# Kernel optimization log

Measured on AMD Instinct MI355X. Metric: run time of the kernel, lower is better.

The kernel has to match this reference:

```python
import jax, jax.numpy as jnp
import numpy as np

LN_EPS = 1e-5
MASK_FILL = -1e9


def setup_inputs() -> dict:
    key = jax.random.key(0)
    ks = jax.random.split(key, 8)
    B, S, D = 32, 1024, 1280
    Dout = 1280
    emb = jax.random.normal(ks[0], (B, S, D), dtype=jnp.float32)
    mask = jnp.ones((B, S), dtype=jnp.int32)
    w = 0.02
    return {
        "embeddings": emb,
        "attention_mask": mask,
        "Wq": jax.random.normal(ks[1], (D, D), jnp.float32) * w,
        "bq": jnp.zeros((D,), jnp.float32),
        "Wk": jax.random.normal(ks[2], (D, D), jnp.float32) * w,
        "bk": jnp.zeros((D,), jnp.float32),
        "Wv": jax.random.normal(ks[3], (D, D), jnp.float32) * w,
        "bv": jnp.zeros((D,), jnp.float32),
        "Wo": jax.random.normal(ks[4], (Dout, D), jnp.float32) * w,
        "bo": jnp.zeros((Dout,), jnp.float32),
        "gamma": jnp.ones((Dout,), jnp.float32),
        "beta": jnp.zeros((Dout,), jnp.float32),
    }


def reference(embeddings, attention_mask, Wq, bq, Wk, bk, Wv, bv, Wo, bo, gamma, beta):
    # Original torch module computes full [B,S,S] self-attention but only
    # consumes context[:, 0, :]. Mathematically identical (same output and
    # same gradients) to computing attention for query row 0 only.
    B, S, D = embeddings.shape
    scale = D ** -0.5
    q0 = embeddings[:, 0, :] @ Wq.T + bq                      # [B, D]
    k = jnp.einsum("bsd,ed->bse", embeddings, Wk) + bk        # [B, S, D]
    v = jnp.einsum("bsd,ed->bse", embeddings, Wv) + bv        # [B, S, D]
    scores = jnp.einsum("bd,bsd->bs", q0, k) * scale          # [B, S]
    scores = jnp.where(attention_mask == 0, MASK_FILL, scores)
    weights = jax.nn.softmax(scores, axis=-1)                 # [B, S]
    ctx = jnp.einsum("bs,bsd->bd", weights, v)                # [B, D]
    # output projection: Linear -> LayerNorm -> ReLU (dropout = identity in eval)
    h = ctx @ Wo.T + bo                                       # [B, Dout]
    mu = jnp.mean(h, axis=-1, keepdims=True)
    var = jnp.mean(jnp.square(h - mu), axis=-1, keepdims=True)
    h = (h - mu) * jax.lax.rsqrt(var + LN_EPS) * gamma + beta
    return jax.nn.relu(h)
```

## Files before the change

### kernel.cpp

```cpp
#include <hip/hip_runtime.h>

constexpr int cB = 32;
constexpr int cS = 1024;
constexpr int cD = 1280;
constexpr int KC = 16;
constexpr int NKC = cD / KC;
constexpr int NNC = cD / 256;

#define LN_EPS 1e-5f
#define MASK_FILL -1e9f
#define SCALE 0.02795084971874737f

__global__ __launch_bounds__(256) void k_dotT(const float* __restrict__ A,
                                              size_t lda,
                                              const float* __restrict__ W,
                                              const float* __restrict__ bias,
                                              float* __restrict__ out) {
    int w = threadIdx.x >> 6, lane = threadIdx.x & 63;
    int gw = blockIdx.x * 4 + w;
    int n = gw >> 1;
    int bh = (gw & 1) * 16;
    int d0 = lane * 4;

    float4 wr[5];
#pragma unroll
    for (int it = 0; it < 5; ++it)
        wr[it] = *reinterpret_cast<const float4*>(W + (size_t)n * cD + it * 256 + d0);
    float bn = bias[n];

#pragma unroll
    for (int bi = 0; bi < 16; ++bi) {
        int b = bh + bi;
        const float* a = A + (size_t)b * lda + d0;
        float4 av[5];
#pragma unroll
        for (int it = 0; it < 5; ++it)
            av[it] = *reinterpret_cast<const float4*>(a + it * 256);
        float dot = 0.f;
#pragma unroll
        for (int it = 0; it < 5; ++it)
            dot += av[it].x * wr[it].x + av[it].y * wr[it].y
                 + av[it].z * wr[it].z + av[it].w * wr[it].w;
#pragma unroll
        for (int off = 32; off; off >>= 1) dot += __shfl_xor(dot, off, 64);
        if (lane == 0) out[b * cD + n] = dot + bn;
    }
}

__global__ __launch_bounds__(256) void k_mm_p1(const float* __restrict__ A,
                                               const float* __restrict__ B,
                                               float* __restrict__ part) {
    int t = threadIdx.x;
    int nc = blockIdx.x % NNC, kc = blockIdx.x / NNC;
    int n0 = nc * 256, k0 = kc * KC;

    float w[KC];
#pragma unroll
    for (int kk = 0; kk < KC; ++kk)
        w[kk] = B[(size_t)(k0 + kk) * cD + n0 + t];

#pragma unroll
    for (int b = 0; b < cB; ++b) {
        const float* Ab = A + (size_t)b * cD + k0;
        float a0 = 0.f, a1 = 0.f, a2 = 0.f, a3 = 0.f;
#pragma unroll
        for (int kk = 0; kk < KC; kk += 4) {
            a0 += Ab[kk + 0] * w[kk + 0];
            a1 += Ab[kk + 1] * w[kk + 1];
            a2 += Ab[kk + 2] * w[kk + 2];
            a3 += Ab[kk + 3] * w[kk + 3];
        }
        part[(size_t)kc * (cB * cD) + b * cD + n0 + t] = (a0 + a1) + (a2 + a3);
    }
}

__global__ __launch_bounds__(256) void k_mm_red_qb(const float* __restrict__ part,
                                                   const float* __restrict__ q0,
                                                   const float* __restrict__ bk,
                                                   float* __restrict__ qk,
                                                   float* __restrict__ qb) {
    if (blockIdx.x < 160) {
        int i = blockIdx.x * 256 + threadIdx.x;
        float s = 0.f;
#pragma unroll
        for (int c = 0; c < NKC; ++c) s += part[(size_t)c * (cB * cD) + i];
        qk[i] = s;
    } else {
        int w = threadIdx.x >> 6, lane = threadIdx.x & 63;
        int d0 = lane * 4;
        float4 bkr[5];
#pragma unroll
        for (int it = 0; it < 5; ++it)
            bkr[it] = *reinterpret_cast<const float4*>(bk + it * 256 + d0);
#pragma unroll
        for (int r = 0; r < 8; ++r) {
            int b = w * 8 + r;
            float dot = 0.f;
#pragma unroll
            for (int it = 0; it < 5; ++it) {
                float4 qv = *reinterpret_cast<const float4*>(q0 + b * cD + it * 256 + d0);
                dot += qv.x * bkr[it].x + qv.y * bkr[it].y
                     + qv.z * bkr[it].z + qv.w * bkr[it].w;
            }
#pragma unroll
            for (int off = 32; off; off >>= 1) dot += __shfl_xor(dot, off, 64);
            if (lane == 0) qb[b] = dot;
        }
    }
}

__global__ __launch_bounds__(256) void k_attn(const float* __restrict__ emb,
                                              const float* __restrict__ qk,
                                              const float* __restrict__ qb,
                                              const int* __restrict__ mask,
                                              float* __restrict__ pm,
                                              float* __restrict__ pl,
                                              float* __restrict__ pacc) {
    __shared__ float s_all[4][cD];
    __shared__ float s_m[4], s_l[4];
    int blk = blockIdx.x;
    int b = blk >> 5, sc = blk & 31;
    int w = threadIdx.x >> 6, lane = threadIdx.x & 63;
    int d0 = lane * 4;

    float4 qkr[5];
#pragma unroll
    for (int it = 0; it < 5; ++it)
        qkr[it] = *reinterpret_cast<const float4*>(qk + b * cD + it * 256 + d0);
    float qbv = qb[b];

    float m = -INFINITY, l = 0.f;
    float4 acc[5];
#pragma unroll
    for (int it = 0; it < 5; ++it) acc[it] = make_float4(0.f, 0.f, 0.f, 0.f);

    int s0 = sc * 32 + w * 8;
    const float* ebase = emb + (size_t)(b * cS + s0) * cD + d0;

#define ATTN_ROW(rIdx, er)                                                     \
    {                                                                          \
        int s = s0 + (rIdx);                                                   \
        float dot = 0.f;                                                       \
        _Pragma("unroll")                                                      \
        for (int it = 0; it < 5; ++it)                                         \
            dot += er[it].x * qkr[it].x + er[it].y * qkr[it].y                 \
                 + er[it].z * qkr[it].z + er[it].w * qkr[it].w;                \
        _Pragma("unroll")                                                      \
        for (int off = 32; off; off >>= 1) dot += __shfl_xor(dot, off, 64);    \
        float scv = (mask[b * cS + s] == 0) ? MASK_FILL : (dot + qbv) * SCALE; \
        if (scv > m) {                                                         \
            float f = __expf(m - scv);                                         \
            l *= f;                                                            \
            _Pragma("unroll")                                                  \
            for (int it = 0; it < 5; ++it) {                                   \
                acc[it].x *= f; acc[it].y *= f;                                \
                acc[it].z *= f; acc[it].w *= f;                                \
            }                                                                  \
            m = scv;                                                           \
        }                                                                      \
        float p = __expf(scv - m);                                             \
        l += p;                                                                \
        _Pragma("unroll")                                                      \
        for (int it = 0; it < 5; ++it) {                                       \
            acc[it].x += p * er[it].x; acc[it].y += p * er[it].y;              \
            acc[it].z += p * er[it].z; acc[it].w += p * er[it].w;              \
        }                                                                      \
    }

    float4 erA[5], erB[5];
#pragma unroll
    for (int it = 0; it < 5; ++it)
        erA[it] = *reinterpret_cast<const float4*>(ebase + it * 256);

#pragma unroll
    for (int rr = 0; rr < 8; rr += 2) {
#pragma unroll
        for (int it = 0; it < 5; ++it)
            erB[it] = *reinterpret_cast<const float4*>(
                ebase + (size_t)(rr + 1) * cD + it * 256);
        ATTN_ROW(rr, erA);
        if (rr + 2 < 8) {
#pragma unroll
            for (int it = 0; it < 5; ++it)
                erA[it] = *reinterpret_cast<const float4*>(
                    ebase + (size_t)(rr + 2) * cD + it * 256);
        }
        ATTN_ROW(rr + 1, erB);
    }
#undef ATTN_ROW

    if (lane == 0) { s_m[w] = m; s_l[w] = l; }
    __syncthreads();
    float M = fmaxf(fmaxf(s_m[0], s_m[1]), fmaxf(s_m[2], s_m[3]));
    float f = __expf(m - M);
#pragma unroll
    for (int it = 0; it < 5; ++it)
        *reinterpret_cast<float4*>(&s_all[w][it * 256 + d0]) =
            make_float4(acc[it].x * f, acc[it].y * f, acc[it].z * f, acc[it].w * f);
    __syncthreads();

    if (threadIdx.x == 0) {
        float lt = s_l[0] * __expf(s_m[0] - M) + s_l[1] * __expf(s_m[1] - M)
                 + s_l[2] * __expf(s_m[2] - M) + s_l[3] * __expf(s_m[3] - M);
        pm[blk] = M; pl[blk] = lt;
    }
#pragma unroll
    for (int j = 0; j < 5; ++j) {
        int d = j * 256 + threadIdx.x;
        pacc[(size_t)blk * cD + d] =
            s_all[0][d] + s_all[1][d] + s_all[2][d] + s_all[3][d];
    }
}

__global__ __launch_bounds__(256) void k_attn_red(const float* __restrict__ pm,
                                                  const float* __restrict__ pl,
                                                  const float* __restrict__ pacc,
                                                  float* __restrict__ ectx) {
    int b = blockIdx.x / 5, j = blockIdx.x % 5;
    int d = j * 256 + threadIdx.x;
    float M = -INFINITY;
    for (int i = 0; i < 32; ++i) M = fmaxf(M, pm[b * 32 + i]);
    float L = 0.f, a = 0.f;
    for (int i = 0; i < 32; ++i) {
        float wf = __expf(pm[b * 32 + i] - M);
        L += pl[b * 32 + i] * wf;
        a += wf * pacc[(size_t)(b * 32 + i) * cD + d];
    }
    ectx[b * cD + d] = a / L;
}

__global__ __launch_bounds__(256) void k_ln(const float* __restrict__ h,
                                            const float* __restrict__ gamma,
                                            const float* __restrict__ beta,
                                            float* __restrict__ out) {
    int b = blockIdx.x;
    __shared__ float red[8];
    int wid = threadIdx.x >> 6, lane = threadIdx.x & 63;
    float v[5];
    float sum = 0.f;
#pragma unroll
    for (int j = 0; j < 5; ++j) {
        v[j] = h[b * cD + threadIdx.x + 256 * j];
        sum += v[j];
    }
#pragma unroll
    for (int off = 32; off; off >>= 1) sum += __shfl_xor(sum, off, 64);
    if (lane == 0) red[wid] = sum;
    __syncthreads();
    float mu = (red[0] + red[1] + red[2] + red[3]) * (1.f / cD);
    float vs = 0.f;
#pragma unroll
    for (int j = 0; j < 5; ++j) { float t = v[j] - mu; vs += t * t; }
#pragma unroll
    for (int off = 32; off; off >>= 1) vs += __shfl_xor(vs, off, 64);
    if (lane == 0) red[4 + wid] = vs;
    __syncthreads();
    float var = (red[4] + red[5] + red[6] + red[7]) * (1.f / cD);
    float inv = rsqrtf(var + LN_EPS);
#pragma unroll
    for (int j = 0; j < 5; ++j) {
        int idx = threadIdx.x + 256 * j;
        float o = (v[j] - mu) * inv * gamma[idx] + beta[idx];
        out[b * cD + idx] = fmaxf(o, 0.f);
    }
}

extern "C" void kernel_launch(void* const* d_in, const int* in_sizes, int n_in,
                              void* d_out, int out_size, void* d_ws, size_t ws_size,
                              hipStream_t stream) {
    const float* emb   = (const float*)d_in[0];
    const int*   mask  = (const int*)d_in[1];
    const float* Wq    = (const float*)d_in[2];
    const float* bq    = (const float*)d_in[3];
    const float* Wk    = (const float*)d_in[4];
    const float* bk    = (const float*)d_in[5];
    const float* Wv    = (const float*)d_in[6];
    const float* bv    = (const float*)d_in[7];
    const float* Wo    = (const float*)d_in[8];
    const float* bo    = (const float*)d_in[9];
    const float* gamma = (const float*)d_in[10];
    const float* beta  = (const float*)d_in[11];

    float* ws   = (float*)d_ws;
    float* part = ws;
    float* q0   = part + NKC * cB * cD;
    float* qk   = q0 + cB * cD;
    float* qb   = qk + cB * cD;
    float* pm   = qb + cB;
    float* pl   = pm + 1024;
    float* pacc = pl + 1024;
    float* ectx = pacc + (size_t)1024 * cD;
    float* ctx  = ectx + cB * cD;
    float* h    = ctx + cB * cD;

    k_dotT<<<640, 256, 0, stream>>>(emb, (size_t)cS * cD, Wq, bq, q0);
    k_mm_p1<<<NNC * NKC, 256, 0, stream>>>(q0, Wk, part);
    k_mm_red_qb<<<161, 256, 0, stream>>>(part, q0, bk, qk, qb);
    k_attn<<<cB * 32, 256, 0, stream>>>(emb, qk, qb, mask, pm, pl, pacc);
    k_attn_red<<<160, 256, 0, stream>>>(pm, pl, pacc, ectx);
    k_dotT<<<640, 256, 0, stream>>>(ectx, (size_t)cD, Wv, bv, ctx);
    k_dotT<<<640, 256, 0, stream>>>(ctx, (size_t)cD, Wo, bo, h);
    k_ln<<<cB, 256, 0, stream>>>(h, gamma, beta, (float*)d_out);
}
```

Measured before the change: 345.2 us.

## Replace split-K q·Wk partial GEMM with direct per-output kernel; batch shuffle reductions

Merges the split-K partial-sum kernel and its reduction into one kernel where each thread computes a full K=1280 dot product for one (batch, column) of q0·Wk. This removes the large partial buffer (80×32×1280 floats) along with its write and readback, and drops one launch. The cost is lower parallelism: only 160 blocks, each running a long serial loop over strided Wk rows. It also batches the warp-shuffle reductions across the 16 and 8 rows in k_dotT and the qb path for more ILP, and adds unroll pragmas in k_attn_red.

Measured after the change: 346.1 us. Within noise of the previous version (+0.3%).

```diff
diff --git a/kernel.cpp b/kernel.cpp
--- a/kernel.cpp
+++ b/kernel.cpp
@@ -3,8 +3,6 @@
 constexpr int cB = 32;
 constexpr int cS = 1024;
 constexpr int cD = 1280;
-constexpr int KC = 16;
-constexpr int NKC = cD / KC;
 constexpr int NNC = cD / 256;
 
 #define LN_EPS 1e-5f
@@ -28,6 +26,7 @@
         wr[it] = *reinterpret_cast<const float4*>(W + (size_t)n * cD + it * 256 + d0);
     float bn = bias[n];
 
+    float dot[16];
 #pragma unroll
     for (int bi = 0; bi < 16; ++bi) {
         int b = bh + bi;
@@ -36,55 +35,50 @@
 #pragma unroll
         for (int it = 0; it < 5; ++it)
             av[it] = *reinterpret_cast<const float4*>(a + it * 256);
-        float dot = 0.f;
+        float d = 0.f;
 #pragma unroll
         for (int it = 0; it < 5; ++it)
-            dot += av[it].x * wr[it].x + av[it].y * wr[it].y
-                 + av[it].z * wr[it].z + av[it].w * wr[it].w;
-#pragma unroll
-        for (int off = 32; off; off >>= 1) dot += __shfl_xor(dot, off, 64);
-        if (lane == 0) out[b * cD + n] = dot + bn;
-    }
-}
-
-__global__ __launch_bounds__(256) void k_mm_p1(const float* __restrict__ A,
-                                               const float* __restrict__ B,
-                                               float* __restrict__ part) {
-    int t = threadIdx.x;
-    int nc = blockIdx.x % NNC, kc = blockIdx.x / NNC;
-    int n0 = nc * 256, k0 = kc * KC;
-
-    float w[KC];
-#pragma unroll
-    for (int kk = 0; kk < KC; ++kk)
-        w[kk] = B[(size_t)(k0 + kk) * cD + n0 + t];
-
-#pragma unroll
-    for (int b = 0; b < cB; ++b) {
-        const float* Ab = A + (size_t)b * cD + k0;
+            d += av[it].x * wr[it].x + av[it].y * wr[it].y
+               + av[it].z * wr[it].z + av[it].w * wr[it].w;
+        dot[bi] = d;
+    }
+#pragma unroll
+    for (int off = 32; off; off >>= 1)
+#pragma unroll
+        for (int bi = 0; bi < 16; ++bi)
+            dot[bi] += __shfl_xor(dot[bi], off, 64);
+    if (lane == 0) {
+#pragma unroll
+        for (int bi = 0; bi < 16; ++bi)
+            out[(bh + bi) * cD + n] = dot[bi] + bn;
+    }
+}
+
+__global__ __launch_bounds__(256) void k_qk(const float* __restrict__ q0,
+                                            const float* __restrict__ Wk,
+                                            const float* __restrict__ bk,
+                                            float* __restrict__ qk,
+                                            float* __restrict__ qb) {
+    if (blockIdx.x < 160) {
+        int b = blockIdx.x / NNC, nc = blockIdx.x % NNC;
+        int n = nc * 256 + threadIdx.x;
+        const float* Ab = q0 + (size_t)b * cD;
+        const float* Wp = Wk + n;
         float a0 = 0.f, a1 = 0.f, a2 = 0.f, a3 = 0.f;
-#pragma unroll
-        for (int kk = 0; kk < KC; kk += 4) {
-            a0 += Ab[kk + 0] * w[kk + 0];
-            a1 += Ab[kk + 1] * w[kk + 1];
-            a2 += Ab[kk + 2] * w[kk + 2];
-            a3 += Ab[kk + 3] * w[kk + 3];
+        float a4 = 0.f, a5 = 0.f, a6 = 0.f, a7 = 0.f;
+        for (int kk = 0; kk < cD; kk += 8) {
+            const float* wrow = Wp + (size_t)kk * cD;
+            a0 += Ab[kk + 0] * wrow[0 * cD];
+            a1 += Ab[kk + 1] * wrow[1 * cD];
+            a2 += Ab[kk + 2] * wrow[2 * cD];
+            a3 += Ab[kk + 3] * wrow[3 * cD];
+            a4 += Ab[kk + 4] * wrow[4 * cD];
+            a5 += Ab[kk + 5] * wrow[5 * cD];
+            a6 += Ab[kk + 6] * wrow[6 * cD];
+            a7 += Ab[kk + 7] * wrow[7 * cD];
         }
-        part[(size_t)kc * (cB * cD) + b * cD + n0 + t] = (a0 + a1) + (a2 + a3);
-    }
-}
-
-__global__ __launch_bounds__(256) void k_mm_red_qb(const float* __restrict__ part,
-                                                   const float* __restrict__ q0,
-                                                   const float* __restrict__ bk,
-                                                   float* __restrict__ qk,
-                                                   float* __restrict__ qb) {
-    if (blockIdx.x < 160) {
-        int i = blockIdx.x * 256 + threadIdx.x;
-        float s = 0.f;
-#pragma unroll
-        for (int c = 0; c < NKC; ++c) s += part[(size_t)c * (cB * cD) + i];
-        qk[i] = s;
+        qk[(size_t)b * cD + n] =
+            ((a0 + a1) + (a2 + a3)) + ((a4 + a5) + (a6 + a7));
     } else {
         int w = threadIdx.x >> 6, lane = threadIdx.x & 63;
         int d0 = lane * 4;
@@ -92,19 +86,27 @@
 #pragma unroll
         for (int it = 0; it < 5; ++it)
             bkr[it] = *reinterpret_cast<const float4*>(bk + it * 256 + d0);
+        float dot[8];
 #pragma unroll
         for (int r = 0; r < 8; ++r) {
             int b = w * 8 + r;
-            float dot = 0.f;
+            float d = 0.f;
 #pragma unroll
             for (int it = 0; it < 5; ++it) {
                 float4 qv = *reinterpret_cast<const float4*>(q0 + b * cD + it * 256 + d0);
-                dot += qv.x * bkr[it].x + qv.y * bkr[it].y
-                     + qv.z * bkr[it].z + qv.w * bkr[it].w;
+                d += qv.x * bkr[it].x + qv.y * bkr[it].y
+                   + qv.z * bkr[it].z + qv.w * bkr[it].w;
             }
-#pragma unroll
-            for (int off = 32; off; off >>= 1) dot += __shfl_xor(dot, off, 64);
-            if (lane == 0) qb[b] = dot;
+            dot[r] = d;
+        }
+#pragma unroll
+        for (int off = 32; off; off >>= 1)
+#pragma unroll
+            for (int r = 0; r < 8; ++r)
+                dot[r] += __shfl_xor(dot[r], off, 64);
+        if (lane == 0) {
+#pragma unroll
+            for (int r = 0; r < 8; ++r) qb[w * 8 + r] = dot[r];
         }
     }
 }
@@ -219,8 +221,10 @@
     int b = blockIdx.x / 5, j = blockIdx.x % 5;
     int d = j * 256 + threadIdx.x;
     float M = -INFINITY;
+#pragma unroll 8
     for (int i = 0; i < 32; ++i) M = fmaxf(M, pm[b * 32 + i]);
     float L = 0.f, a = 0.f;
+#pragma unroll 8
     for (int i = 0; i < 32; ++i) {
         float wf = __expf(pm[b * 32 + i] - M);
         L += pl[b * 32 + i] * wf;
@@ -282,8 +286,7 @@
     const float* beta  = (const float*)d_in[11];
 
     float* ws   = (float*)d_ws;
-    float* part = ws;
-    float* q0   = part + NKC * cB * cD;
+    float* q0   = ws;
     float* qk   = q0 + cB * cD;
     float* qb   = qk + cB * cD;
     float* pm   = qb + cB;
@@ -294,8 +297,7 @@
     float* h    = ctx + cB * cD;
 
     k_dotT<<<640, 256, 0, stream>>>(emb, (size_t)cS * cD, Wq, bq, q0);
-    k_mm_p1<<<NNC * NKC, 256, 0, stream>>>(q0, Wk, part);
-    k_mm_red_qb<<<161, 256, 0, stream>>>(part, q0, bk, qk, qb);
+    k_qk<<<161, 256, 0, stream>>>(q0, Wk, bk, qk, qb);
     k_attn<<<cB * 32, 256, 0, stream>>>(emb, qk, qb, mask, pm, pl, pacc);
     k_attn_red<<<160, 256, 0, stream>>>(pm, pl, pacc, ectx);
     k_dotT<<<640, 256, 0, stream>>>(ectx, (size_t)cD, Wv, bv, ctx);
```
